# Performance work log

Hardware: AMD Instinct MI355X
Metric: run time of the kernel (lower is better)

## Reference

```python
import jax, jax.numpy as jnp
import numpy as np

B, C_HR, C_LR, HH, WH, HL, WL = 2, 256, 256, 128, 128, 64, 64
CC = 64            # compressed channels
LK, HK, EK = 5, 3, 3
GROUPS, LW, SCALE = 4, 3, 2


def conv2d(x, w, b, pad, dilation=1):
    out = jax.lax.conv_general_dilated(
        x, w, (1, 1), [(pad, pad), (pad, pad)],
        rhs_dilation=(dilation, dilation),
        dimension_numbers=('NCHW', 'OIHW', 'NCHW'))
    return out + b[None, :, None, None]


def unfold(x, k, dilation=1):
    # torch F.unfold with padding=(k//2)*dilation -> [B,C,k*k,H,W], row-major kernel order
    pad = (k // 2) * dilation
    Bb, C, H, W = x.shape
    xp = jnp.pad(x, ((0, 0), (0, 0), (pad, pad), (pad, pad)))
    patches = [xp[:, :, i * dilation:i * dilation + H, j * dilation:j * dilation + W]
               for i in range(k) for j in range(k)]
    return jnp.stack(patches, axis=2)


def kernel_normalizer(mask, k, hamming):
    n, c, h, w = mask.shape
    mc = c // (k * k)
    m = jax.nn.softmax(mask.reshape(n, mc, k * k, h, w), axis=2)
    m = m.reshape(n, mc, k, k, h, w) * hamming[None, None, :, :, None, None]
    m = m / jnp.sum(m, axis=(2, 3), keepdims=True)
    return m.reshape(n, c, h, w)


def carafe(feat, mask, k, scale):
    # mmcv CARAFE with group=1: mask at output resolution [B,k*k,H*s,W*s]
    Bb, C, H, W = feat.shape
    unf = unfold(feat, k)  # [B,C,k2,H,W]
    if scale == 1:
        return jnp.einsum('bckhw,bkhw->bchw', unf, mask)
    m = mask.reshape(Bb, k * k, H, scale, W, scale)
    out = jnp.einsum('bckhw,bkhpwq->bchpwq', unf, m)
    return out.reshape(Bb, C, H * scale, W * scale)


def group_norm(x, gamma, beta, groups, eps=1e-5):
    Bb, C, H, W = x.shape
    xg = x.reshape(Bb, groups, -1)
    mu = xg.mean(-1, keepdims=True)
    var = xg.var(-1, keepdims=True)
    xn = ((xg - mu) * jax.lax.rsqrt(var + eps)).reshape(Bb, C, H, W)
    return xn * gamma[None, :, None, None] + beta[None, :, None, None]


def compute_similarity(x, k=LW, dilation=2):
    unf = unfold(x, k, dilation)  # [B,C,k2,H,W]
    c = k * k // 2
    center = unf[:, :, c:c + 1]
    eps = 1e-8
    num = jnp.sum(center * unf, axis=1)
    den = (jnp.maximum(jnp.linalg.norm(center, axis=1), eps)
           * jnp.maximum(jnp.linalg.norm(unf, axis=1), eps))
    sim = num / den  # [B,k2,H,W]
    return jnp.concatenate([sim[:, :c], sim[:, c + 1:]], axis=1)


def pixel_shuffle(x, r):
    Bb, C, H, W = x.shape
    x = x.reshape(Bb, C // (r * r), r, r, H, W)
    return x.transpose(0, 1, 4, 2, 5, 3).reshape(Bb, C // (r * r), H * r, W * r)


def pixel_unshuffle(x, r):
    Bb, C, H, W = x.shape
    x = x.reshape(Bb, C, H // r, r, W // r, r)
    return x.transpose(0, 1, 3, 5, 2, 4).reshape(Bb, C * r * r, H // r, W // r)


def grid_sample_border(x, grid):
    # bilinear, padding_mode='border', align_corners=False; grid [N,Hg,Wg,2] (x,y)
    N, C, H, W = x.shape
    gx = jnp.clip((grid[..., 0] + 1.0) * W * 0.5 - 0.5, 0.0, W - 1.0)
    gy = jnp.clip((grid[..., 1] + 1.0) * H * 0.5 - 0.5, 0.0, H - 1.0)
    x0 = jnp.floor(gx); y0 = jnp.floor(gy)
    tx = (gx - x0)[:, None]; ty = (gy - y0)[:, None]
    x0i = x0.astype(jnp.int32); y0i = y0.astype(jnp.int32)
    x1i = jnp.minimum(x0i + 1, W - 1); y1i = jnp.minimum(y0i + 1, H - 1)
    g = jax.vmap(lambda img, yi, xi: img[:, yi, xi])
    v00 = g(x, y0i, x0i); v01 = g(x, y0i, x1i)
    v10 = g(x, y1i, x0i); v11 = g(x, y1i, x1i)
    return (v00 * (1 - tx) * (1 - ty) + v01 * tx * (1 - ty)
            + v10 * (1 - tx) * ty + v11 * tx * ty)


def init_pos():
    h = jnp.arange((-SCALE + 1) / 2, (SCALE - 1) / 2 + 1) / SCALE  # [-0.25, 0.25]
    t = jnp.stack(jnp.meshgrid(h, h, indexing='ij'))
    t = jnp.transpose(t, (0, 2, 1))
    return jnp.tile(t, (1, GROUPS, 1)).reshape(1, -1, 1, 1).astype(jnp.float32)


def dysampler(hr_x, lr_x, feat, gn_hr_w, gn_hr_b, gn_lr_w, gn_lr_b,
              w_off, b_off, w_hoff, b_hoff, w_ds, b_ds, w_hds, b_hds):
    hr_x = group_norm(hr_x, gn_hr_w, gn_hr_b, CC // 8)
    lr_x = group_norm(lr_x, gn_lr_w, gn_lr_b, CC // 8)
    hr_sim = compute_similarity(hr_x)
    lr_sim = compute_similarity(lr_x)
    pad = EK // 2
    off = conv2d(lr_sim, w_off, b_off, pad) + pixel_unshuffle(conv2d(hr_sim, w_hoff, b_hoff, pad), SCALE)
    ds = conv2d(lr_x, w_ds, b_ds, pad) + pixel_unshuffle(conv2d(hr_x, w_hds, b_hds, pad), SCALE)
    offset = off * jax.nn.sigmoid(ds) + init_pos()  # [B, 2*G*s^2, Hl, Wl]
    Bb, _, H, W = offset.shape
    off5 = offset.reshape(Bb, 2, -1, H, W)
    cw = jnp.arange(W, dtype=offset.dtype) + 0.5
    ch = jnp.arange(H, dtype=offset.dtype) + 0.5
    base = jnp.stack([jnp.broadcast_to(cw[None, :], (H, W)),
                      jnp.broadcast_to(ch[:, None], (H, W))])  # [2,H,W] (x,y)
    norm = jnp.array([W, H], offset.dtype).reshape(1, 2, 1, 1, 1)
    coords = 2.0 * (base[None, :, None] + off5) / norm - 1.0  # [B,2,G*s^2,H,W]
    coords = pixel_shuffle(coords.reshape(Bb, -1, H, W), SCALE)  # [B,2*G,sH,sW]
    coords = (coords.reshape(Bb, 2, GROUPS, SCALE * H, SCALE * W)
              .transpose(0, 2, 3, 4, 1)
              .reshape(Bb * GROUPS, SCALE * H, SCALE * W, 2))
    xs = feat.reshape(Bb * GROUPS, -1, feat.shape[-2], feat.shape[-1])
    out = grid_sample_border(xs, coords)
    return out.reshape(Bb, -1, SCALE * H, SCALE * W)


def setup_inputs() -> dict:
    key = jax.random.key(0)
    ks = jax.random.split(key, 16)
    r = lambda i, shape, s=0.05: jax.random.normal(ks[i], shape, jnp.float32) * s
    LC2, HC2 = LK * LK, HK * HK
    SIMC = LW * LW - 1
    OC = 2 * GROUPS * SCALE * SCALE
    OCH = 2 * GROUPS
    return {
        'hr_feat': jax.random.normal(ks[0], (B, C_HR, HH, WH), jnp.float32),
        'lr_feat': jax.random.normal(ks[1], (B, C_LR, HL, WL), jnp.float32),
        'w_hr_comp': r(2, (CC, C_HR, 1, 1)), 'b_hr_comp': r(3, (CC,)),
        'w_lr_comp': r(4, (CC, C_LR, 1, 1)), 'b_lr_comp': r(5, (CC,)),
        'w_enc': r(6, (LC2, CC, EK, EK), 0.01), 'b_enc': r(7, (LC2,), 0.01),
        'w_enc2': r(8, (HC2, CC, EK, EK), 0.01), 'b_enc2': r(9, (HC2,), 0.01),
        'gn_hr_w': jnp.ones((CC,), jnp.float32), 'gn_hr_b': jnp.zeros((CC,), jnp.float32),
        'gn_lr_w': jnp.ones((CC,), jnp.float32), 'gn_lr_b': jnp.zeros((CC,), jnp.float32),
        'w_off': r(10, (OC, SIMC, EK, EK), 0.01), 'b_off': jnp.zeros((OC,), jnp.float32),
        'w_hoff': r(11, (OCH, SIMC, EK, EK), 0.01), 'b_hoff': jnp.zeros((OCH,), jnp.float32),
        'w_ds': r(12, (OC, CC, EK, EK), 0.01), 'b_ds': jnp.zeros((OC,), jnp.float32),
        'w_hds': r(13, (OCH, CC, EK, EK), 0.01), 'b_hds': jnp.zeros((OCH,), jnp.float32),
    }


def reference(hr_feat, lr_feat, w_hr_comp, b_hr_comp, w_lr_comp, b_lr_comp,
              w_enc, b_enc, w_enc2, b_enc2, gn_hr_w, gn_hr_b, gn_lr_w, gn_lr_b,
              w_off, b_off, w_hoff, b_hoff, w_ds, b_ds, w_hds, b_hds):
    ham_lo = jnp.asarray(np.outer(np.hamming(LK), np.hamming(LK)), jnp.float32)
    ham_hi = jnp.asarray(np.outer(np.hamming(HK), np.hamming(HK)), jnp.float32)
    epad = EK // 2
    ch = conv2d(hr_feat, w_hr_comp, b_hr_comp, 0)
    cl = conv2d(lr_feat, w_lr_comp, b_lr_comp, 0)
    # semi_conv + comp_feat_upsample + use_high_pass path
    mask_hr_hr = conv2d(ch, w_enc2, b_enc2, epad)
    mh_init = kernel_normalizer(mask_hr_hr, HK, ham_hi)
    ch = 2.0 * ch - carafe(ch, mh_init, HK, 1)
    mask_lr_hr = conv2d(ch, w_enc, b_enc, epad)
    ml_init = kernel_normalizer(mask_lr_hr, LK, ham_lo)
    mask_lr_lr = carafe(conv2d(cl, w_enc, b_enc, epad), ml_init, LK, 2)
    mask_lr = mask_lr_hr + mask_lr_lr
    ml_init2 = kernel_normalizer(mask_lr, LK, ham_lo)
    mask_hr_lr = carafe(conv2d(cl, w_enc2, b_enc2, epad), ml_init2, LK, 2)
    mask_hr = mask_hr_hr + mask_hr_lr
    mask_lr_n = kernel_normalizer(mask_lr, LK, ham_lo)
    lr_up = carafe(lr_feat, mask_lr_n, LK, 2)
    mask_hr_n = kernel_normalizer(mask_hr, HK, ham_hi)
    hr_out = 2.0 * hr_feat - carafe(hr_feat, mask_hr_n, HK, 1)  # hr_residual
    lr_out = dysampler(ch, cl, lr_up, gn_hr_w, gn_hr_b, gn_lr_w, gn_lr_b,
                       w_off, b_off, w_hoff, b_hoff, w_ds, b_ds, w_hds, b_hds)
    return mask_lr_n, hr_out, lr_out
```

## Files before the change

### kernel.cpp

```cpp
#include <hip/hip_runtime.h>
#include <hip/hip_bf16.h>

typedef __hip_bfloat16 bf16;
#define TPB 256

__device__ __forceinline__ float toF(float v){ return v; }
__device__ __forceinline__ float toF(bf16 v){ return __bfloat162float(v); }
__device__ __forceinline__ float bfu(unsigned short u){
    unsigned int x = ((unsigned int)u) << 16;
    return __uint_as_float(x);
}
template<typename T> __device__ __forceinline__ void stT(T* p, long i, float v);
template<> __device__ __forceinline__ void stT<float>(float* p, long i, float v){ p[i] = v; }
template<> __device__ __forceinline__ void stT<bf16>(bf16* p, long i, float v){ p[i] = __float2bfloat16(v); }

__device__ __forceinline__ void st4bf(bf16* p, const float* a){
    bf16 t0 = __float2bfloat16(a[0]);
    bf16 t1 = __float2bfloat16(a[1]);
    bf16 t2 = __float2bfloat16(a[2]);
    bf16 t3 = __float2bfloat16(a[3]);
    ushort4 pk;
    pk.x = *(unsigned short*)&t0;
    pk.y = *(unsigned short*)&t1;
    pk.z = *(unsigned short*)&t2;
    pk.w = *(unsigned short*)&t3;
    *(ushort4*)p = pk;
}

static inline int nblk(long n){ return (int)((n + TPB - 1) / TPB); }

__global__ void k_detect(const void* hr, int n, int* flag, float* stat)
{
    if (threadIdx.x < 64) stat[threadIdx.x] = 0.f;
    const unsigned short* u = (const unsigned short*)hr;
    int nan = 0, oz = 0, ot = 0;
    for (int i = threadIdx.x; i < n; i += TPB) {
        unsigned short a = u[i] & 0x7FFF;
        if (a >= 0x7F80) nan++;
        if (i & 1) { ot++; if (a == 0) oz++; }
    }
    __shared__ int s1[TPB], s2[TPB], s3[TPB];
    s1[threadIdx.x] = nan; s2[threadIdx.x] = oz; s3[threadIdx.x] = ot;
    __syncthreads();
    if (threadIdx.x == 0) {
        int a = 0, b = 0, c = 0;
        for (int i = 0; i < TPB; i++) { a += s1[i]; b += s2[i]; c += s3[i]; }
        *flag = (a >= 6 || (long)b * 10 >= (long)c * 9) ? 1 : 0;
    }
}

#define P_W_HRC 0
#define P_B_HRC 16384
#define P_W_LRC 16448
#define P_B_LRC 32832
#define P_W_ENC 32896
#define P_B_ENC 47296
#define P_W_ENC2 47321
#define P_B_ENC2 52505
#define P_GNHW 52514
#define P_GNHB 52578
#define P_GNLW 52642
#define P_GNLB 52706
#define P_W_OFF 52770
#define P_B_OFF 55074
#define P_W_HOFF 55106
#define P_B_HOFF 55682
#define P_W_DS 55690
#define P_B_DS 74122
#define P_W_HDS 74154
#define P_B_HDS 78762
#define P_TOT 78770

__constant__ int c_segsz[20]  = {16384,64,16384,64,14400,25,5184,9,64,64,64,64,2304,32,576,8,18432,32,4608,8};
__constant__ int c_segbase[20]= {P_W_HRC,P_B_HRC,P_W_LRC,P_B_LRC,P_W_ENC,P_B_ENC,P_W_ENC2,P_B_ENC2,
                                 P_GNHW,P_GNHB,P_GNLW,P_GNLB,P_W_OFF,P_B_OFF,P_W_HOFF,P_B_HOFF,
                                 P_W_DS,P_B_DS,P_W_HDS,P_B_HDS};
__constant__ int c_segcin[20] = {256,0,256,0, 64,0, 64,0, 0,0,0,0, 8,0, 8,0, 64,0, 64,0};
__constant__ int c_segcout[20]= { 64,0, 64,0, 25,0,  9,0, 0,0,0,0,32,0, 8,0, 32,0,  8,0};
__constant__ int c_segtap[20] = {  1,0,  1,0,  9,0,  9,0, 0,0,0,0, 9,0, 9,0,  9,0,  9,0};

__global__ void k_prep(const void* p0,const void* p1,const void* p2,const void* p3,
                       const void* p4,const void* p5,const void* p6,const void* p7,
                       const void* p8,const void* p9,const void* p10,const void* p11,
                       const void* p12,const void* p13,const void* p14,const void* p15,
                       const void* p16,const void* p17,const void* p18,const void* p19,
                       float* dst, const int* flag)
{
    int idx = blockIdx.x * TPB + threadIdx.x;
    if (idx >= P_TOT) return;
    int s = 0, off = idx;
    while (off >= c_segsz[s]) { off -= c_segsz[s]; s++; }
    const void* sp;
    switch (s) {
        case 0: sp=p0; break;  case 1: sp=p1; break;  case 2: sp=p2; break;  case 3: sp=p3; break;
        case 4: sp=p4; break;  case 5: sp=p5; break;  case 6: sp=p6; break;  case 7: sp=p7; break;
        case 8: sp=p8; break;  case 9: sp=p9; break;  case 10: sp=p10; break; case 11: sp=p11; break;
        case 12: sp=p12; break; case 13: sp=p13; break; case 14: sp=p14; break; case 15: sp=p15; break;
        case 16: sp=p16; break; case 17: sp=p17; break; case 18: sp=p18; break; default: sp=p19; break;
    }
    float v = (*flag) ? ((const float*)sp)[off] : toF(((const bf16*)sp)[off]);
    int doff = off;
    int cin = c_segcin[s];
    if (cin) {
        int t = c_segtap[s], cout = c_segcout[s];
        int co = off / (cin * t);
        int r  = off % (cin * t);
        int ci = r / t, k = r % t;
        doff = (ci * cout + co) * t + k;
    }
    dst[c_segbase[s] + doff] = v;
}

template<typename T>
__device__ void transpLR_body(const T* __restrict__ x, bf16* __restrict__ xT, int Bn)
{
    __shared__ float tile[64][65];
    int bid = blockIdx.x;
    int pg = bid & 63;
    int cg = (bid >> 6) & 3;
    int b  = bid >> 8;
    int tid = threadIdx.x;
    int tr = tid >> 6, tc = tid & 63;
    for (int i = 0; i < 16; i++) {
        int c = tr + i * 4;
        tile[c][tc] = toF(x[(((long)(b * 256 + cg * 64 + c)) << 12) + (pg << 6) + tc]);
    }
    __syncthreads();
    for (int i = 0; i < 16; i++) {
        int p = tr + i * 4;
        xT[((((long)b << 12) + (pg << 6) + p) << 8) + (cg << 6) + tc] = __float2bfloat16(tile[tc][p]);
    }
}
__global__ void k_transpLR(const void* x, bf16* xT, int Bn, const int* flag)
{
    if (*flag) transpLR_body<float>((const float*)x, xT, Bn);
    else       transpLR_body<bf16 >((const bf16*)x,  xT, Bn);
}

__global__ void k_carafe5T(const bf16* __restrict__ featT, const float* __restrict__ mask,
                           bf16* __restrict__ outT, int Bn)
{
    int lane = threadIdx.x & 63;
    int nwg = gridDim.x;
    int bid = blockIdx.x;
    int swz = (nwg & 7) ? bid : ((bid & 7) * (nwg >> 3) + (bid >> 3));
    int wid = (swz << 2) | (threadIdx.x >> 6);
    wid = __builtin_amdgcn_readfirstlane(wid);
    if (wid >= Bn * 4096) return;
    int ipix = wid & 4095;
    int b    = wid >> 12;
    int h = ipix >> 6, w = ipix & 63;
    const bf16*  fb = featT + (((long)b << 12) << 8) + (lane << 2);
    const float* mb = mask + (((long)b * 25) << 14) + (h << 8) + (w << 1);
    float a00[4], a01[4], a10[4], a11[4];
    #pragma unroll
    for (int t = 0; t < 4; t++) { a00[t]=0.f; a01[t]=0.f; a10[t]=0.f; a11[t]=0.f; }
    #pragma unroll
    for (int k = 0; k < 25; k++) {
        const int i = k / 5, j = k % 5;
        int yy = h + i - 2, xx = w + j - 2;
        bool v = (yy >= 0 && yy < 64 && xx >= 0 && xx < 64);
        int yc = v ? yy : 0, xc = v ? xx : 0;
        ushort4 u = *(const ushort4*)(fb + ((long)((yc << 6) + xc) << 8));
        float2 mr0 = *(const float2*)(mb + ((long)k << 14));
        float2 mr1 = *(const float2*)(mb + ((long)k << 14) + 128);
        float m00 = v ? mr0.x : 0.f, m01 = v ? mr0.y : 0.f;
        float m10 = v ? mr1.x : 0.f, m11 = v ? mr1.y : 0.f;
        float f0 = bfu(u.x), f1 = bfu(u.y), f2 = bfu(u.z), f3 = bfu(u.w);
        a00[0] += f0*m00; a00[1] += f1*m00; a00[2] += f2*m00; a00[3] += f3*m00;
        a01[0] += f0*m01; a01[1] += f1*m01; a01[2] += f2*m01; a01[3] += f3*m01;
        a10[0] += f0*m10; a10[1] += f1*m10; a10[2] += f2*m10; a10[3] += f3*m10;
        a11[0] += f0*m11; a11[1] += f1*m11; a11[2] += f2*m11; a11[3] += f3*m11;
    }
    bf16* op = outT + (((long)(b << 14) + (h << 8) + (w << 1)) << 8) + (lane << 2);
    st4bf(op, a00);
    st4bf(op + 256, a01);
    st4bf(op + (128 << 8), a10);
    st4bf(op + (128 << 8) + 256, a11);
}

template<int COUT>
__global__ void k_conv3x3p(const float* __restrict__ x, const float* __restrict__ wf,
                           float* __restrict__ pbuf, int Bn, int CIN, int H, int W, int CS)
{
    int HW = H * W;
    int idx = blockIdx.x * TPB + threadIdx.x;
    if (idx >= Bn * HW) return;
    int chunk = blockIdx.y;
    int pix = idx % HW, b = idx / HW;
    int wx = pix % W, hy = pix / W;
    int off[9]; float msk[9];
    #pragma unroll
    for (int i = 0; i < 3; i++) {
        int yy = hy + i - 1; bool vy = (yy >= 0 && yy < H); int yc = vy ? yy : hy;
        #pragma unroll
        for (int j = 0; j < 3; j++) {
            int xx = wx + j - 1; bool v = vy && (xx >= 0 && xx < W);
            int xc = (xx >= 0 && xx < W) ? xx : wx;
            off[i*3+j] = yc * W + xc; msk[i*3+j] = v ? 1.f : 0.f;
        }
    }
    float acc[COUT];
    #pragma unroll
    for (int co = 0; co < COUT; co++) acc[co] = 0.f;
    int c0 = chunk * CS;
    const float* xb = x + ((long)b * CIN + c0) * HW;
    const float* wb = wf + (long)c0 * COUT * 9;
    #pragma unroll 2
    for (int ci = 0; ci < CS; ci++) {
        const float* xc = xb + (long)ci * HW;
        float t[9];
        #pragma unroll
        for (int k = 0; k < 9; k++) t[k] = xc[off[k]] * msk[k];
        const float* wr = wb + (long)ci * COUT * 9;
        #pragma unroll
        for (int co = 0; co < COUT; co++) {
            const float* wp = wr + co * 9;
            acc[co] += t[0]*wp[0] + t[1]*wp[1] + t[2]*wp[2] + t[3]*wp[3] + t[4]*wp[4]
                     + t[5]*wp[5] + t[6]*wp[6] + t[7]*wp[7] + t[8]*wp[8];
        }
    }
    long pb = ((long)chunk * Bn + b) * COUT * (long)HW + pix;
    #pragma unroll
    for (int co = 0; co < COUT; co++) pbuf[pb + (long)co * HW] = acc[co];
}

__global__ void k_convr(const float* __restrict__ pbuf, const float* __restrict__ bias,
                        float* __restrict__ out, int Bn, int COUT, int HW, int nChunk)
{
    long idx = (long)blockIdx.x * TPB + threadIdx.x;
    if (idx >= (long)Bn * COUT * HW) return;
    int pix = idx % HW;
    int co  = (idx / HW) % COUT;
    int b   = idx / ((long)HW * COUT);
    float v = bias[co];
    for (int ch = 0; ch < nChunk; ch++)
        v += pbuf[(((long)ch * Bn + b) * COUT + co) * HW + pix];
    out[idx] = v;
}

template<typename T>
__device__ void conv1x1p_body(const T* __restrict__ x, const float* __restrict__ wf,
                              float* __restrict__ pbuf, int Bn, int CIN, int HW, int CS)
{
    int idx = blockIdx.x * TPB + threadIdx.x;
    if (idx >= Bn * HW) return;
    int chunk = blockIdx.y;
    int pix = idx % HW, b = idx / HW;
    float acc[64];
    #pragma unroll
    for (int co = 0; co < 64; co++) acc[co] = 0.f;
    int c0 = chunk * CS;
    const T* xp = x + ((long)b * CIN + c0) * HW + pix;
    const float* wb = wf + (long)c0 * 64;
    #pragma unroll 2
    for (int ci = 0; ci < CS; ci++) {
        float v = toF(xp[(long)ci * HW]);
        const float* wr = wb + ci * 64;
        #pragma unroll
        for (int co = 0; co < 64; co++) acc[co] += v * wr[co];
    }
    long pb = ((long)chunk * Bn + b) * 64 * (long)HW + pix;
    #pragma unroll
    for (int co = 0; co < 64; co++) pbuf[pb + (long)co * HW] = acc[co];
}
__global__ void k_conv1x1p(const void* x, const float* wf, float* pbuf,
                           int Bn, int CIN, int HW, int CS, const int* flag)
{
    if (*flag) conv1x1p_body<float>((const float*)x, wf, pbuf, Bn, CIN, HW, CS);
    else       conv1x1p_body<bf16 >((const bf16*)x,  wf, pbuf, Bn, CIN, HW, CS);
}

template<int K, typename OT>
__device__ void knorm_body(const float* __restrict__ mask, float* __restrict__ out,
                           OT* __restrict__ outb, int B, int H, int W)
{
    const int K2 = K * K;
    int HWi = H * W;
    int idx = blockIdx.x * TPB + threadIdx.x;
    if (idx >= B * HWi) return;
    int pix = idx % HWi;
    int b   = idx / HWi;
    long HW = (long)HWi;
    long base = (long)b * K2 * HW + pix;
    float v[K2];
    float m = -1e30f;
    for (int k = 0; k < K2; k++) { v[k] = mask[base + k*HW]; m = fmaxf(m, v[k]); }
    float s2 = 0.f;
    for (int k = 0; k < K2; k++) {
        int i = k / K, j = k % K;
        float hi = (K == 3) ? ((i==1)?1.f:0.08f) : ((i==2)?1.f:((i==1||i==3)?0.54f:0.08f));
        float hj = (K == 3) ? ((j==1)?1.f:0.08f) : ((j==2)?1.f:((j==1||j==3)?0.54f:0.08f));
        v[k] = expf(v[k] - m) * hi * hj;
        s2 += v[k];
    }
    float inv = 1.f / s2;
    for (int k = 0; k < K2; k++) {
        float r = v[k] * inv;
        out[base + k*HW] = r;
        if (outb) stT<OT>(outb, base + k*HW, r);
    }
}
template<int K>
__global__ void k_knorm(const float* mask, float* out, void* outb, int B, int H, int W, const int* flag)
{
    if (*flag) knorm_body<K, float>(mask, out, (float*)outb, B, H, W);
    else       knorm_body<K, bf16>(mask, out, (bf16*)outb, B, H, W);
}

template<typename TF, typename TO, int NC>
__device__ void carafe3c_body(const TF* __restrict__ feat, const float* __restrict__ mask,
                              TO* __restrict__ out, int Bn)
{
    constexpr int CH = NC / 8;
    int idx = blockIdx.x * TPB + threadIdx.x;
    if (idx >= Bn * CH * 16384) return;
    int px = idx & 16383;
    int cc = (idx >> 14) % CH;
    int b  = (idx >> 14) / CH;
    int wx = px & 127, hy = px >> 7;
    float mk[9]; int off[9];
    #pragma unroll
    for (int i = 0; i < 3; i++) {
        int yy = hy + i - 1; bool vy = (yy >= 0 && yy < 128); int yc = vy ? yy : hy;
        #pragma unroll
        for (int j = 0; j < 3; j++) {
            int xx = wx + j - 1; bool v = vy && (xx >= 0 && xx < 128);
            int xc = (xx >= 0 && xx < 128) ? xx : wx;
            int k = i*3 + j;
            float m = mask[(((long)b*9 + k) << 14) + px];
            mk[k] = v ? m : 0.f;
            off[k] = (yc << 7) + xc;
        }
    }
    long base = ((long)(b * NC + cc * 8) << 14);
    for (int c = 0; c < 8; c++) {
        const TF* fp = feat + base + ((long)c << 14);
        float ctr = 0.f, acc = 0.f;
        #pragma unroll
        for (int k = 0; k < 9; k++) {
            float v = toF(fp[off[k]]);
            if (k == 4) ctr = v;
            acc += v * mk[k];
        }
        stT<TO>(out, base + ((long)c << 14) + px, 2.f * ctr - acc);
    }
}
__global__ void k_carafe3c_ws(const float* feat, const float* mask, float* out, int Bn)
{
    carafe3c_body<float, float, 64>(feat, mask, out, Bn);
}
__global__ void k_carafe3c_io(const void* feat, const float* mask, void* out, long outOff,
                              int Bn, const int* flag)
{
    if (*flag) carafe3c_body<float, float, 256>((const float*)feat, mask, (float*)out + outOff, Bn);
    else       carafe3c_body<bf16, bf16, 256>((const bf16*)feat, mask, (bf16*)out + outOff, Bn);
}

template<typename TF, typename TO, bool ADD, int CG>
__device__ void carafe5_body(const TF* __restrict__ feat, const float* __restrict__ mask,
                             const float* __restrict__ add, TO* __restrict__ out,
                             int Bn, int C)
{
    int ng = C / CG;
    int idx = blockIdx.x * TPB + threadIdx.x;
    if (idx >= Bn * ng * 16384) return;
    int px = idx & 16383;
    int gi = (idx >> 14) % ng;
    int b  = (idx >> 14) / ng;
    int X = px & 127, Y = px >> 7;
    int h = Y >> 1, w = X >> 1;
    float mk[25]; int off[25];
    const float* mb = mask + (((long)b * 25) << 14) + px;
    #pragma unroll
    for (int i = 0; i < 5; i++) {
        int yy = h + i - 2; bool vy = (yy >= 0 && yy < 64); int yc = vy ? yy : 0;
        #pragma unroll
        for (int j = 0; j < 5; j++) {
            int xx = w + j - 2; bool v = vy && (xx >= 0 && xx < 64);
            int xc = (xx >= 0 && xx < 64) ? xx : 0;
            int k = i*5 + j;
            mk[k] = v ? mb[(long)k << 14] : 0.f;
            off[k] = (yc << 6) + xc;
        }
    }
    int c0 = gi * CG;
    for (int c = 0; c < CG; c++) {
        long fb = ((long)(b * C + c0 + c) << 12);
        long ob = ((long)(b * C + c0 + c) << 14) + px;
        const TF* fp = feat + fb;
        float acc = ADD ? add[ob] : 0.f;
        #pragma unroll
        for (int k = 0; k < 25; k++) acc += toF(fp[off[k]]) * mk[k];
        stT<TO>(out, ob, acc);
    }
}
template<int CG>
__global__ void k_carafe5_ws(const float* feat, const float* mask, const float* add,
                             float* out, int Bn, int C)
{
    carafe5_body<float, float, true, CG>(feat, mask, add, out, Bn, C);
}

__global__ void k_gnstat(const float* __restrict__ x, float* __restrict__ stat, int statBase,
                         int S, int N)
{
    int bid = blockIdx.x;
    int bg = bid / S, sl = bid % S;
    int seg = N / S;
    long base = (long)bg * N + (long)sl * seg;
    float s = 0.f, ss = 0.f;
    for (int i = threadIdx.x; i < seg; i += TPB) {
        float v = x[base + i]; s += v; ss += v * v;
    }
    __shared__ float sh[8];
    for (int off = 32; off; off >>= 1) { s += __shfl_down(s, off); ss += __shfl_down(ss, off); }
    int wave = threadIdx.x >> 6, lane = threadIdx.x & 63;
    if (lane == 0) { sh[wave] = s; sh[4 + wave] = ss; }
    __syncthreads();
    if (threadIdx.x == 0) {
        float ts = 0.f, tss = 0.f;
        for (int i = 0; i < TPB/64; i++) { ts += sh[i]; tss += sh[4 + i]; }
        atomicAdd(&stat[statBase + bg*2], ts);
        atomicAdd(&stat[statBase + bg*2 + 1], tss);
    }
}
__global__ void k_gnapply(const float* __restrict__ x, const float* __restrict__ stat, int statBase,
                          const float* __restrict__ gamma, const float* __restrict__ beta,
                          float* __restrict__ out, int G, int Cg, int HW, int Bn)
{
    long idx = (long)blockIdx.x * TPB + threadIdx.x;
    long total = (long)Bn * G * Cg * HW;
    if (idx >= total) return;
    int bgN = Cg * HW;
    int bg = idx / bgN;
    int r  = idx % bgN;
    int g = bg % G;
    int c = g * Cg + r / HW;
    float s = stat[statBase + bg*2], ss = stat[statBase + bg*2 + 1];
    float mean = s / bgN;
    float inv = rsqrtf(ss / bgN - mean * mean + 1e-5f);
    out[idx] = (x[idx] - mean) * inv * gamma[c] + beta[c];
}

__global__ void k_simp(const float* __restrict__ x, float* __restrict__ pbuf,
                       int Bn, int H, int W, int CS)
{
    int HW = H * W;
    int idx = blockIdx.x * TPB + threadIdx.x;
    if (idx >= Bn * HW) return;
    int chunk = blockIdx.y;
    int pix = idx % HW, b = idx / HW;
    int wx = pix % W, hy = pix / W;
    const int dyv[8] = {-2,-2,-2, 0, 0, 2, 2, 2};
    const int dxv[8] = {-2, 0, 2,-2, 2,-2, 0, 2};
    int off[8]; float msk[8];
    #pragma unroll
    for (int n = 0; n < 8; n++) {
        int yy = hy + dyv[n], xx = wx + dxv[n];
        bool v = (yy >= 0 && yy < H && xx >= 0 && xx < W);
        off[n] = v ? yy * W + xx : pix;
        msk[n] = v ? 1.f : 0.f;
    }
    float dc = 0.f, num[8], dn[8];
    #pragma unroll
    for (int n = 0; n < 8; n++) { num[n] = 0.f; dn[n] = 0.f; }
    const float* xb = x + ((long)b * 64 + chunk * CS) * HW;
    #pragma unroll 2
    for (int ci = 0; ci < CS; ci++) {
        const float* xc = xb + (long)ci * HW;
        float c0 = xc[pix];
        dc += c0 * c0;
        #pragma unroll
        for (int n = 0; n < 8; n++) {
            float v = xc[off[n]] * msk[n];
            num[n] += c0 * v; dn[n] += v * v;
        }
    }
    long base = ((long)chunk * Bn + b) * 17 * (long)HW + pix;
    pbuf[base] = dc;
    #pragma unroll
    for (int n = 0; n < 8; n++) {
        pbuf[base + (long)(1 + n) * HW] = num[n];
        pbuf[base + (long)(9 + n) * HW] = dn[n];
    }
}
__global__ void k_simr(const float* __restrict__ pbuf, float* __restrict__ out,
                       int Bn, int HW, int nChunk)
{
    int idx = blockIdx.x * TPB + threadIdx.x;
    if (idx >= Bn * HW) return;
    int pix = idx % HW, b = idx / HW;
    float dc = 0.f, num[8], dn[8];
    #pragma unroll
    for (int n = 0; n < 8; n++) { num[n] = 0.f; dn[n] = 0.f; }
    for (int ch = 0; ch < nChunk; ch++) {
        long base = ((long)ch * Bn + b) * 17 * (long)HW + pix;
        dc += pbuf[base];
        #pragma unroll
        for (int n = 0; n < 8; n++) {
            num[n] += pbuf[base + (long)(1 + n) * HW];
            dn[n]  += pbuf[base + (long)(9 + n) * HW];
        }
    }
    float nc = fmaxf(sqrtf(dc), 1e-8f);
    #pragma unroll
    for (int n = 0; n < 8; n++)
        out[((long)(b*8 + n)) * HW + pix] = num[n] / (nc * fmaxf(sqrtf(dn[n]), 1e-8f));
}

__global__ void k_offset(const float* __restrict__ lro, const float* __restrict__ hro,
                         const float* __restrict__ lrd, const float* __restrict__ hrd,
                         float* __restrict__ outoff, int B)
{
    int idx = blockIdx.x * TPB + threadIdx.x;
    int total = B * 32 * 64 * 64;
    if (idx >= total) return;
    int wx = idx & 63;
    int hy = (idx >> 6) & 63;
    int o  = (idx >> 12) & 31;
    int b  = idx >> 17;
    int c = o >> 2, p = (o >> 1) & 1, q = o & 1;
    long hridx = ((long)(b*8 + c) * 128 + 2*hy + p) * 128 + 2*wx + q;
    float off = lro[idx] + hro[hridx];
    float dsv = lrd[idx] + hrd[hridx];
    float sg = 1.f / (1.f + expf(-dsv));
    int comp = o >> 4;
    float ip = (comp == 0) ? (q ? 0.25f : -0.25f) : (p ? 0.25f : -0.25f);
    outoff[idx] = off * sg + ip;
}

template<typename OT>
__device__ void gridsampleT_body(const unsigned short* __restrict__ lrupT,
                                 const float* __restrict__ offb, OT* __restrict__ out, int Bn)
{
    int idx = blockIdx.x * TPB + threadIdx.x;
    if (idx >= Bn * 4 * 16384) return;
    int ch0 = blockIdx.y << 5;
    int opix = idx & 16383;
    int g = (idx >> 14) & 3, b = idx >> 16;
    int X = opix & 127, Y = opix >> 7;
    int h = Y >> 1, p = Y & 1, w = X >> 1, q = X & 1;
    int r = g*4 + p*2 + q;
    float offx = offb[((long)(b*32 + r)      << 12) + (h << 6) + w];
    float offy = offb[((long)(b*32 + 16 + r) << 12) + (h << 6) + w];
    float gx = fminf(fmaxf(2.f * (w + 0.5f + offx) - 0.5f, 0.f), 127.f);
    float gy = fminf(fmaxf(2.f * (h + 0.5f + offy) - 0.5f, 0.f), 127.f);
    float x0f = floorf(gx), y0f = floorf(gy);
    float tx = gx - x0f, ty = gy - y0f;
    int x0 = (int)x0f, y0 = (int)y0f;
    int x1 = min(x0 + 1, 127), y1 = min(y0 + 1, 127);
    float w11 = tx * ty, w10 = ty - w11, w01 = tx - w11, w00 = 1.f - tx - ty + w11;
    const unsigned short* base = lrupT + (((long)b << 14) << 8) + (g << 6) + ch0;
    long a00 = ((long)((y0 << 7) + x0)) << 8, a01 = ((long)((y0 << 7) + x1)) << 8;
    long a10 = ((long)((y1 << 7) + x0)) << 8, a11 = ((long)((y1 << 7) + x1)) << 8;
    OT* op = out + ((long)(b * 256 + g * 64 + ch0) << 14) + opix;
    #pragma unroll
    for (int c8 = 0; c8 < 4; c8++) {
        uint4 v00 = *(const uint4*)(base + a00 + c8*8);
        uint4 v01 = *(const uint4*)(base + a01 + c8*8);
        uint4 v10 = *(const uint4*)(base + a10 + c8*8);
        uint4 v11 = *(const uint4*)(base + a11 + c8*8);
        const unsigned short* u00 = (const unsigned short*)&v00;
        const unsigned short* u01 = (const unsigned short*)&v01;
        const unsigned short* u10 = (const unsigned short*)&v10;
        const unsigned short* u11 = (const unsigned short*)&v11;
        #pragma unroll
        for (int t = 0; t < 8; t++) {
            float res = bfu(u00[t])*w00 + bfu(u01[t])*w01 + bfu(u10[t])*w10 + bfu(u11[t])*w11;
            stT<OT>(op, ((long)(c8*8 + t) << 14), res);
        }
    }
}
__global__ void k_gridsampleT(const bf16* lrupT, const float* offb, void* out, long outOff,
                              int Bn, const int* flag)
{
    if (*flag) gridsampleT_body<float>((const unsigned short*)lrupT, offb, (float*)out + outOff, Bn);
    else       gridsampleT_body<bf16 >((const unsigned short*)lrupT, offb, (bf16*)out + outOff, Bn);
}

extern "C" void kernel_launch(void* const* d_in, const int* in_sizes, int n_in,
                              void* d_out, int out_size, void* d_ws, size_t ws_size,
                              hipStream_t stream) {
    const void* hr_feat = d_in[0];
    const void* lr_feat = d_in[1];

    const int B = 2, HH = 128, HL = 64;
    const int HWH = HH*HH, HWL = HL*HL;

    int*   flag = (int*)d_ws;
    float* stat = (float*)d_ws + 4;
    float* P    = (float*)d_ws + 80;
    float* ws   = P + ((P_TOT + 63) & ~63);

    size_t o = 0;
    float* ch0    = ws + o; o += (size_t)B*64*HWH;
    float* clb    = ws + o; o += (size_t)B*64*HWL;
    float* maskHH = ws + o; o += (size_t)B*9*HWH;
    float* tmp9   = ws + o; o += (size_t)B*9*HWH;
    float* chn    = ws + o; o += (size_t)B*64*HWH;
    float* m25a   = ws + o; o += (size_t)B*25*HWH;
    float* m25b   = ws + o; o += (size_t)B*25*HWH;
    float* m25c   = ws + o; o += (size_t)B*25*HWH;
    float* enccl  = ws + o; o += (size_t)B*25*HWL;
    float* enc2cl = ws + o; o += (size_t)B*9*HWL;
    bf16*  lrupT  = (bf16*)(ws + o); o += (size_t)B*256*HWH/2;
    float* lrx    = ws + o; o += (size_t)B*64*HWL;
    float* hrsim  = ws + o; o += (size_t)B*8*HWH;
    float* lrsim  = ws + o; o += (size_t)B*8*HWL;
    float* qhro   = ws + o; o += (size_t)B*8*HWH;
    float* qlro   = ws + o; o += (size_t)B*32*HWL;
    float* qhrd   = ws + o; o += (size_t)B*8*HWH;
    float* qlrd   = ws + o; o += (size_t)B*32*HWL;
    float* offb   = ws + o; o += (size_t)B*32*HWL;
    float* hrx   = ch0;
    float* maskH = m25b;
    float* pbufA  = maskHH;
    float* pbuf3  = tmp9;
    float* pbuf6  = m25b;
    float* pbufL8 = (float*)lrupT;
    float* pbufT  = chn;
    bf16*  lrfT   = (bf16*)hrsim;
    (void)ws_size; (void)n_in;

    long out1Off = (long)B*25*HWH;
    long out2Off = out1Off + (long)B*256*HWH;

    const float* pw_hrc = P + P_W_HRC;  const float* pb_hrc = P + P_B_HRC;
    const float* pw_lrc = P + P_W_LRC;  const float* pb_lrc = P + P_B_LRC;
    const float* pw_enc = P + P_W_ENC;  const float* pb_enc = P + P_B_ENC;
    const float* pw_enc2= P + P_W_ENC2; const float* pb_enc2= P + P_B_ENC2;
    const float* pgnhw  = P + P_GNHW;   const float* pgnhb  = P + P_GNHB;
    const float* pgnlw  = P + P_GNLW;   const float* pgnlb  = P + P_GNLB;
    const float* pw_off = P + P_W_OFF;  const float* pb_off = P + P_B_OFF;
    const float* pw_hoff= P + P_W_HOFF; const float* pb_hoff= P + P_B_HOFF;
    const float* pw_ds  = P + P_W_DS;   const float* pb_ds  = P + P_B_DS;
    const float* pw_hds = P + P_W_HDS;  const float* pb_hds = P + P_B_HDS;

    int nDet = in_sizes[0] < 16384 ? in_sizes[0] : 16384;
    k_detect<<<1, TPB, 0, stream>>>(hr_feat, nDet, flag, stat);
    k_prep<<<nblk(P_TOT), TPB, 0, stream>>>(d_in[2],d_in[3],d_in[4],d_in[5],d_in[6],d_in[7],
        d_in[8],d_in[9],d_in[10],d_in[11],d_in[12],d_in[13],d_in[14],d_in[15],d_in[16],
        d_in[17],d_in[18],d_in[19],d_in[20],d_in[21], P, flag);
    k_transpLR<<<B*4*64, TPB, 0, stream>>>(lr_feat, lrfT, B, flag);

    k_conv1x1p<<<dim3(nblk((long)B*HWH),4), TPB, 0, stream>>>(hr_feat, pw_hrc, pbufA, B, 256, HWH, 64, flag);
    k_convr<<<nblk((long)B*64*HWH), TPB, 0, stream>>>(pbufA, pb_hrc, ch0, B, 64, HWH, 4);
    k_conv1x1p<<<dim3(nblk((long)B*HWL),16), TPB, 0, stream>>>(lr_feat, pw_lrc, pbufA, B, 256, HWL, 16, flag);
    k_convr<<<nblk((long)B*64*HWL), TPB, 0, stream>>>(pbufA, pb_lrc, clb, B, 64, HWL, 16);
    k_conv3x3p<9><<<dim3(nblk((long)B*HWH),8), TPB, 0, stream>>>(ch0, pw_enc2, pbuf3, B, 64, HH, HH, 8);
    k_convr<<<nblk((long)B*9*HWH), TPB, 0, stream>>>(pbuf3, pb_enc2, maskHH, B, 9, HWH, 8);
    k_knorm<3><<<nblk((long)B*HWH), TPB, 0, stream>>>(maskHH, tmp9, nullptr, B, HH, HH, flag);
    k_carafe3c_ws<<<nblk((long)B*8*16384), TPB, 0, stream>>>(ch0, tmp9, chn, B);
    k_conv3x3p<25><<<dim3(nblk((long)B*HWH),8), TPB, 0, stream>>>(chn, pw_enc, pbuf6, B, 64, HH, HH, 8);
    k_convr<<<nblk((long)B*25*HWH), TPB, 0, stream>>>(pbuf6, pb_enc, m25a, B, 25, HWH, 8);
    k_knorm<5><<<nblk((long)B*HWH), TPB, 0, stream>>>(m25a, m25b, nullptr, B, HH, HH, flag);
    k_conv3x3p<25><<<dim3(nblk((long)B*HWL),16), TPB, 0, stream>>>(clb, pw_enc, pbufL8, B, 64, HL, HL, 4);
    k_convr<<<nblk((long)B*25*HWL), TPB, 0, stream>>>(pbufL8, pb_enc, enccl, B, 25, HWL, 16);
    k_carafe5_ws<5><<<nblk((long)B*5*16384), TPB, 0, stream>>>(enccl, m25b, m25a, m25c, B, 25);
    k_knorm<5><<<nblk((long)B*HWH), TPB, 0, stream>>>(m25c, m25a, d_out, B, HH, HH, flag);
    k_conv3x3p<9><<<dim3(nblk((long)B*HWL),16), TPB, 0, stream>>>(clb, pw_enc2, pbufL8, B, 64, HL, HL, 4);
    k_convr<<<nblk((long)B*9*HWL), TPB, 0, stream>>>(pbufL8, pb_enc2, enc2cl, B, 9, HWL, 16);
    k_carafe5_ws<3><<<nblk((long)B*3*16384), TPB, 0, stream>>>(enc2cl, m25a, maskHH, maskH, B, 9);
    k_knorm<3><<<nblk((long)B*HWH), TPB, 0, stream>>>(maskH, tmp9, nullptr, B, HH, HH, flag);
    k_carafe3c_io<<<nblk((long)B*32*16384), TPB, 0, stream>>>(hr_feat, tmp9, d_out, out1Off, B, flag);
    k_carafe5T<<<B*4096/4, TPB, 0, stream>>>(lrfT, m25a, lrupT, B);
    k_gnstat<<<16*32, TPB, 0, stream>>>(chn, stat, 0, 32, 8*HWH);
    k_gnapply<<<nblk((long)B*64*HWH), TPB, 0, stream>>>(chn, stat, 0, pgnhw, pgnhb, hrx, 8, 8, HWH, B);
    k_gnstat<<<16*8, TPB, 0, stream>>>(clb, stat, 32, 8, 8*HWL);
    k_gnapply<<<nblk((long)B*64*HWL), TPB, 0, stream>>>(clb, stat, 32, pgnlw, pgnlb, lrx, 8, 8, HWL, B);
    k_simp<<<dim3(nblk((long)B*HWH),8), TPB, 0, stream>>>(hrx, pbufT, B, HH, HH, 8);
    k_simr<<<nblk((long)B*HWH), TPB, 0, stream>>>(pbufT, hrsim, B, HWH, 8);
    k_simp<<<dim3(nblk((long)B*HWL),16), TPB, 0, stream>>>(lrx, pbufT, B, HL, HL, 4);
    k_simr<<<nblk((long)B*HWL), TPB, 0, stream>>>(pbufT, lrsim, B, HWL, 16);
    k_conv3x3p<8><<<dim3(nblk((long)B*HWH),4), TPB, 0, stream>>>(hrsim, pw_hoff, pbufT, B, 8, HH, HH, 2);
    k_convr<<<nblk((long)B*8*HWH), TPB, 0, stream>>>(pbufT, pb_hoff, qhro, B, 8, HWH, 4);
    k_conv3x3p<32><<<dim3(nblk((long)B*HWL),8), TPB, 0, stream>>>(lrsim, pw_off, pbufT, B, 8, HL, HL, 1);
    k_convr<<<nblk((long)B*32*HWL), TPB, 0, stream>>>(pbufT, pb_off, qlro, B, 32, HWL, 8);
    k_conv3x3p<8><<<dim3(nblk((long)B*HWH),8), TPB, 0, stream>>>(hrx, pw_hds, pbufT, B, 64, HH, HH, 8);
    k_convr<<<nblk((long)B*8*HWH), TPB, 0, stream>>>(pbufT, pb_hds, qhrd, B, 8, HWH, 8);
    k_conv3x3p<32><<<dim3(nblk((long)B*HWL),16), TPB, 0, stream>>>(lrx, pw_ds, pbufT, B, 64, HL, HL, 4);
    k_convr<<<nblk((long)B*32*HWL), TPB, 0, stream>>>(pbufT, pb_ds, qlrd, B, 32, HWL, 16);
    k_offset<<<nblk((long)B*32*HWL), TPB, 0, stream>>>(qlro, qhro, qlrd, qhrd, offb, B);
    k_gridsampleT<<<dim3(nblk((long)B*4*HWH),2), TPB, 0, stream>>>(lrupT, offb, d_out, out2Off, B, flag);
}
```

Baseline: 571.2 us.

## Split 1x1 compression conv over output-channel groups instead of input-channel chunks

The two 1x1 compression convolutions now parallelise over groups of output channels instead of splitting the input channels into chunks. Each thread covers the full 256-channel reduction for CG output channels and writes the biased result directly, so the partial-sum buffer and the separate reduction kernel are gone. Block ids are remapped so that blocks sharing the same pixels land close together in the launch order, which should improve L2 reuse of the input. The trade-off is that each group of blocks re-reads the same input activations, and each thread runs a longer serial loop.

```diff
diff --git a/kernel.cpp b/kernel.cpp
--- a/kernel.cpp
+++ b/kernel.cpp
@@ -239,36 +239,42 @@
     out[idx] = v;
 }
 
-template<typename T>
-__device__ void conv1x1p_body(const T* __restrict__ x, const float* __restrict__ wf,
-                              float* __restrict__ pbuf, int Bn, int CIN, int HW, int CS)
-{
-    int idx = blockIdx.x * TPB + threadIdx.x;
+template<typename T, int CG>
+__device__ void conv1x1_body(const T* __restrict__ x, const float* __restrict__ wf,
+                             const float* __restrict__ bias, float* __restrict__ out,
+                             int Bn, int CIN, int HW)
+{
+    constexpr int NG = 64 / CG;
+    int nwg = gridDim.x;
+    int bid = blockIdx.x;
+    int lid = (nwg & 7) ? bid : ((bid & 7) * (nwg >> 3) + (bid >> 3));
+    int grp = lid % NG;
+    int pixblk = lid / NG;
+    int idx = pixblk * TPB + threadIdx.x;
     if (idx >= Bn * HW) return;
-    int chunk = blockIdx.y;
     int pix = idx % HW, b = idx / HW;
-    float acc[64];
-    #pragma unroll
-    for (int co = 0; co < 64; co++) acc[co] = 0.f;
-    int c0 = chunk * CS;
-    const T* xp = x + ((long)b * CIN + c0) * HW + pix;
-    const float* wb = wf + (long)c0 * 64;
-    #pragma unroll 2
-    for (int ci = 0; ci < CS; ci++) {
+    const T* xp = x + (long)b * CIN * HW + pix;
+    const float* wb = wf + grp * CG;
+    float acc[CG];
+    #pragma unroll
+    for (int c = 0; c < CG; c++) acc[c] = 0.f;
+    #pragma unroll 4
+    for (int ci = 0; ci < CIN; ci++) {
         float v = toF(xp[(long)ci * HW]);
         const float* wr = wb + ci * 64;
         #pragma unroll
-        for (int co = 0; co < 64; co++) acc[co] += v * wr[co];
-    }
-    long pb = ((long)chunk * Bn + b) * 64 * (long)HW + pix;
-    #pragma unroll
-    for (int co = 0; co < 64; co++) pbuf[pb + (long)co * HW] = acc[co];
-}
-__global__ void k_conv1x1p(const void* x, const float* wf, float* pbuf,
-                           int Bn, int CIN, int HW, int CS, const int* flag)
-{
-    if (*flag) conv1x1p_body<float>((const float*)x, wf, pbuf, Bn, CIN, HW, CS);
-    else       conv1x1p_body<bf16 >((const bf16*)x,  wf, pbuf, Bn, CIN, HW, CS);
+        for (int c = 0; c < CG; c++) acc[c] += v * wr[c];
+    }
+    long ob = ((long)b * 64 + grp * CG) * HW + pix;
+    #pragma unroll
+    for (int c = 0; c < CG; c++) out[ob + (long)c * HW] = acc[c] + bias[grp * CG + c];
+}
+template<int CG>
+__global__ void k_conv1x1(const void* x, const float* wf, const float* bias, float* out,
+                          int Bn, int CIN, int HW, const int* flag)
+{
+    if (*flag) conv1x1_body<float, CG>((const float*)x, wf, bias, out, Bn, CIN, HW);
+    else       conv1x1_body<bf16, CG>((const bf16*)x,  wf, bias, out, Bn, CIN, HW);
 }
 
 template<int K, typename OT>
@@ -615,7 +621,6 @@
     float* offb   = ws + o; o += (size_t)B*32*HWL;
     float* hrx   = ch0;
     float* maskH = m25b;
-    float* pbufA  = maskHH;
     float* pbuf3  = tmp9;
     float* pbuf6  = m25b;
     float* pbufL8 = (float*)lrupT;
@@ -644,10 +649,8 @@
         d_in[17],d_in[18],d_in[19],d_in[20],d_in[21], P, flag);
     k_transpLR<<<B*4*64, TPB, 0, stream>>>(lr_feat, lrfT, B, flag);
 
-    k_conv1x1p<<<dim3(nblk((long)B*HWH),4), TPB, 0, stream>>>(hr_feat, pw_hrc, pbufA, B, 256, HWH, 64, flag);
-    k_convr<<<nblk((long)B*64*HWH), TPB, 0, stream>>>(pbufA, pb_hrc, ch0, B, 64, HWH, 4);
-    k_conv1x1p<<<dim3(nblk((long)B*HWL),16), TPB, 0, stream>>>(lr_feat, pw_lrc, pbufA, B, 256, HWL, 16, flag);
-    k_convr<<<nblk((long)B*64*HWL), TPB, 0, stream>>>(pbufA, pb_lrc, clb, B, 64, HWL, 16);
+    k_conv1x1<8><<<nblk((long)B*HWH) * 8, TPB, 0, stream>>>(hr_feat, pw_hrc, pb_hrc, ch0, B, 256, HWH, flag);
+    k_conv1x1<2><<<nblk((long)B*HWL) * 32, TPB, 0, stream>>>(lr_feat, pw_lrc, pb_lrc, clb, B, 256, HWL, flag);
     k_conv3x3p<9><<<dim3(nblk((long)B*HWH),8), TPB, 0, stream>>>(ch0, pw_enc2, pbuf3, B, 64, HH, HH, 8);
     k_convr<<<nblk((long)B*9*HWH), TPB, 0, stream>>>(pbuf3, pb_enc2, maskHH, B, 9, HWH, 8);
     k_knorm<3><<<nblk((long)B*HWH), TPB, 0, stream>>>(maskHH, tmp9, nullptr, B, HH, HH, flag);
```

Result: slower. 604.3 us (+5.8%).

## Replace split-K 3x3 convs on high-res maps with shared-memory tiled conv

Applied to the files above, without the earlier changes.

Adds a 3x3 convolution kernel that stages 16x16 output tiles plus halo for 8 input channels at a time in double-buffered shared memory. Each thread computes a small group of output channels over all 64 inputs, with bias added directly. It replaces three split-K conv + reduce kernel pairs on the 128x128 maps, which removes the partial-sum buffer traffic and one launch per conv. The trade-off is less parallelism per pixel and repeated weight reads from global memory per output-channel group. The kernel also assumes H and W are multiples of 16 and exactly 64 input channels.

```diff
diff --git a/kernel.cpp b/kernel.cpp
--- a/kernel.cpp
+++ b/kernel.cpp
@@ -269,6 +269,90 @@
 {
     if (*flag) conv1x1p_body<float>((const float*)x, wf, pbuf, Bn, CIN, HW, CS);
     else       conv1x1p_body<bf16 >((const bf16*)x,  wf, pbuf, Bn, CIN, HW, CS);
+}
+
+template<int CG>
+__global__ __launch_bounds__(256, 2)
+void k_conv3x3t(const float* __restrict__ x, const float* __restrict__ wf,
+                const float* __restrict__ bias, float* __restrict__ out,
+                int H, int W, int COUT)
+{
+    constexpr int CB = 8;
+    constexpr int NE = CB * 324;
+    constexpr int NL = (NE + 255) / 256;
+    __shared__ float s[2][CB][18][18];
+    int tpr = W >> 4;
+    int tpi = (H >> 4) * tpr;
+    int tile = blockIdx.x;
+    int b  = tile / tpi;
+    int t  = tile % tpi;
+    int r0  = (t / tpr) << 4;
+    int c0p = (t % tpr) << 4;
+    int cog = blockIdx.y;
+    int HW = H * W;
+    int tid = threadIdx.x;
+    int row = tid >> 4, col = tid & 15;
+    const float* xb = x + (long)b * 64 * HW;
+
+    float r[NL];
+    float acc[CG];
+    #pragma unroll
+    for (int c = 0; c < CG; c++) acc[c] = 0.f;
+
+    auto LOAD = [&](int cbase) {
+        #pragma unroll
+        for (int k = 0; k < NL; k++) {
+            int e = tid + (k << 8);
+            int ci  = e / 324;
+            int rem = e - ci * 324;
+            int rr = rem / 18, cc = rem - rr * 18;
+            int gr = r0 - 1 + rr, gc = c0p - 1 + cc;
+            bool v = (e < NE) && (gr >= 0) && (gr < H) && (gc >= 0) && (gc < W);
+            r[k] = v ? xb[(long)(cbase + ci) * HW + gr * W + gc] : 0.f;
+        }
+    };
+    auto WRITE = [&](int buf) {
+        #pragma unroll
+        for (int k = 0; k < NL; k++) {
+            int e = tid + (k << 8);
+            if (e < NE) ((float*)s[buf])[e] = r[k];
+        }
+    };
+
+    LOAD(0);
+    WRITE(0);
+    __syncthreads();
+
+    #pragma unroll
+    for (int st = 0; st < 8; st++) {
+        if (st < 7) LOAD((st + 1) * CB);
+        int buf = st & 1;
+        #pragma unroll
+        for (int ci = 0; ci < CB; ci++) {
+            float t0 = s[buf][ci][row  ][col  ], t1 = s[buf][ci][row  ][col+1], t2 = s[buf][ci][row  ][col+2];
+            float t3 = s[buf][ci][row+1][col  ], t4 = s[buf][ci][row+1][col+1], t5 = s[buf][ci][row+1][col+2];
+            float t6 = s[buf][ci][row+2][col  ], t7 = s[buf][ci][row+2][col+1], t8 = s[buf][ci][row+2][col+2];
+            const float* wr = wf + ((long)(st * CB + ci) * COUT + cog * CG) * 9;
+            #pragma unroll
+            for (int c = 0; c < CG; c++) {
+                const float* wp = wr + c * 9;
+                acc[c] += t0*wp[0] + t1*wp[1] + t2*wp[2] + t3*wp[3] + t4*wp[4]
+                        + t5*wp[5] + t6*wp[6] + t7*wp[7] + t8*wp[8];
+            }
+        }
+        if (st < 7) {
+            __syncthreads();
+            WRITE(buf ^ 1);
+            __syncthreads();
+        }
+    }
+
+    int pp = (r0 + row) * W + c0p + col;
+    #pragma unroll
+    for (int c = 0; c < CG; c++) {
+        int co = cog * CG + c;
+        out[((long)b * COUT + co) * HW + pp] = acc[c] + bias[co];
+    }
 }
 
 template<int K, typename OT>
@@ -616,8 +700,6 @@
     float* hrx   = ch0;
     float* maskH = m25b;
     float* pbufA  = maskHH;
-    float* pbuf3  = tmp9;
-    float* pbuf6  = m25b;
     float* pbufL8 = (float*)lrupT;
     float* pbufT  = chn;
     bf16*  lrfT   = (bf16*)hrsim;
@@ -648,12 +730,10 @@
     k_convr<<<nblk((long)B*64*HWH), TPB, 0, stream>>>(pbufA, pb_hrc, ch0, B, 64, HWH, 4);
     k_conv1x1p<<<dim3(nblk((long)B*HWL),16), TPB, 0, stream>>>(lr_feat, pw_lrc, pbufA, B, 256, HWL, 16, flag);
     k_convr<<<nblk((long)B*64*HWL), TPB, 0, stream>>>(pbufA, pb_lrc, clb, B, 64, HWL, 16);
-    k_conv3x3p<9><<<dim3(nblk((long)B*HWH),8), TPB, 0, stream>>>(ch0, pw_enc2, pbuf3, B, 64, HH, HH, 8);
-    k_convr<<<nblk((long)B*9*HWH), TPB, 0, stream>>>(pbuf3, pb_enc2, maskHH, B, 9, HWH, 8);
+    k_conv3x3t<3><<<dim3(B*64,3), TPB, 0, stream>>>(ch0, pw_enc2, pb_enc2, maskHH, HH, HH, 9);
     k_knorm<3><<<nblk((long)B*HWH), TPB, 0, stream>>>(maskHH, tmp9, nullptr, B, HH, HH, flag);
     k_carafe3c_ws<<<nblk((long)B*8*16384), TPB, 0, stream>>>(ch0, tmp9, chn, B);
-    k_conv3x3p<25><<<dim3(nblk((long)B*HWH),8), TPB, 0, stream>>>(chn, pw_enc, pbuf6, B, 64, HH, HH, 8);
-    k_convr<<<nblk((long)B*25*HWH), TPB, 0, stream>>>(pbuf6, pb_enc, m25a, B, 25, HWH, 8);
+    k_conv3x3t<5><<<dim3(B*64,5), TPB, 0, stream>>>(chn, pw_enc, pb_enc, m25a, HH, HH, 25);
     k_knorm<5><<<nblk((long)B*HWH), TPB, 0, stream>>>(m25a, m25b, nullptr, B, HH, HH, flag);
     k_conv3x3p<25><<<dim3(nblk((long)B*HWL),16), TPB, 0, stream>>>(clb, pw_enc, pbufL8, B, 64, HL, HL, 4);
     k_convr<<<nblk((long)B*25*HWL), TPB, 0, stream>>>(pbufL8, pb_enc, enccl, B, 25, HWL, 16);
@@ -677,8 +757,7 @@
     k_convr<<<nblk((long)B*8*HWH), TPB, 0, stream>>>(pbufT, pb_hoff, qhro, B, 8, HWH, 4);
     k_conv3x3p<32><<<dim3(nblk((long)B*HWL),8), TPB, 0, stream>>>(lrsim, pw_off, pbufT, B, 8, HL, HL, 1);
     k_convr<<<nblk((long)B*32*HWL), TPB, 0, stream>>>(pbufT, pb_off, qlro, B, 32, HWL, 8);
-    k_conv3x3p<8><<<dim3(nblk((long)B*HWH),8), TPB, 0, stream>>>(hrx, pw_hds, pbufT, B, 64, HH, HH, 8);
-    k_convr<<<nblk((long)B*8*HWH), TPB, 0, stream>>>(pbufT, pb_hds, qhrd, B, 8, HWH, 8);
+    k_conv3x3t<2><<<dim3(B*64,4), TPB, 0, stream>>>(hrx, pw_hds, pb_hds, qhrd, HH, HH, 8);
     k_conv3x3p<32><<<dim3(nblk((long)B*HWL),16), TPB, 0, stream>>>(lrx, pw_ds, pbufT, B, 64, HL, HL, 4);
     k_convr<<<nblk((long)B*32*HWL), TPB, 0, stream>>>(pbufT, pb_ds, qlrd, B, 32, HWL, 16);
     k_offset<<<nblk((long)B*32*HWL), TPB, 0, stream>>>(qlro, qhro, qlrd, qhrd, offb, B);
```

Result: slower. 971.9 us (+70.2%).
